# Kernel tuning notes

Measured on AMD Instinct MI355X. Metric: run time of the kernel, lower is better.

## Reference

```python
import jax, jax.numpy as jnp
import numpy as np

N_NODES = 50000


def _gcn_conv(x, src, dst, deg_inv_sqrt, W, b, n_nodes):
    # PyG GCNConv: linear transform, then symmetric-normalized aggregation.
    xw = x @ W  # [N, out_dim]
    norm = deg_inv_sqrt[src] * deg_inv_sqrt[dst]  # [E]
    msg = xw[src] * norm[:, None]  # [E, out_dim] gathered messages
    out = jax.ops.segment_sum(msg, dst, num_segments=n_nodes)
    return out + b


def setup_inputs() -> dict:
    key = jax.random.key(0)
    ks = jax.random.split(key, 10)
    n, d_in, d_h, d_z = N_NODES, 128, 128, 64
    e = 800000
    x = jax.random.normal(ks[0], (n, d_in), dtype=jnp.float32)
    edge_index = jax.random.randint(ks[1], (2, e), 0, n, dtype=jnp.int64)
    eps = jax.random.normal(ks[2], (n, d_z), dtype=jnp.float32)
    s_in = 1.0 / np.sqrt(d_in)
    s_h = 1.0 / np.sqrt(d_h)
    W1 = jax.random.normal(ks[3], (d_in, d_h), dtype=jnp.float32) * s_in
    b1 = jnp.zeros((d_h,), dtype=jnp.float32)
    Wmu = jax.random.normal(ks[4], (d_h, d_z), dtype=jnp.float32) * s_h
    bmu = jnp.zeros((d_z,), dtype=jnp.float32)
    Wls = jax.random.normal(ks[5], (d_h, d_z), dtype=jnp.float32) * s_h
    bls = jnp.zeros((d_z,), dtype=jnp.float32)
    return {"x": x, "edge_index": edge_index, "eps": eps,
            "W1": W1, "b1": b1, "Wmu": Wmu, "bmu": bmu, "Wls": Wls, "bls": bls}


def reference(x, edge_index, eps, W1, b1, Wmu, bmu, Wls, bls):
    n = x.shape[0]
    loops = jnp.arange(n, dtype=edge_index.dtype)
    src = jnp.concatenate([edge_index[0], loops])  # add self-loops
    dst = jnp.concatenate([edge_index[1], loops])
    deg = jax.ops.segment_sum(jnp.ones_like(dst, dtype=x.dtype), dst, num_segments=n)
    deg_inv_sqrt = jnp.where(deg > 0, jax.lax.rsqrt(deg), 0.0)

    hidden = jax.nn.relu(_gcn_conv(x, src, dst, deg_inv_sqrt, W1, b1, n))
    mu = _gcn_conv(hidden, src, dst, deg_inv_sqrt, Wmu, bmu, n)
    logstd = _gcn_conv(hidden, src, dst, deg_inv_sqrt, Wls, bls, n)
    z = mu + eps * jnp.exp(logstd)  # reparameterize (training mode)
    return (z, mu, logstd)
```

## Files before the change

kernel.cpp:

```cpp
#include <hip/hip_runtime.h>
#include <math.h>

#define LDP 136
#define EPB 4096
#define BCAP 8192

typedef short v8s __attribute__((ext_vector_type(8)));
typedef float f32x4 __attribute__((ext_vector_type(4)));

static __device__ __forceinline__ unsigned short f2bf(float f) {
    unsigned u = __builtin_bit_cast(unsigned, f);
    return (unsigned short)((u + 0x7FFFu + ((u >> 16) & 1u)) >> 16);
}
static __device__ __forceinline__ float bf_lo(unsigned u) {
    return __builtin_bit_cast(float, u << 16);
}
static __device__ __forceinline__ float bf_hi(unsigned u) {
    return __builtin_bit_cast(float, u & 0xFFFF0000u);
}

__global__ void prep_w(const float* __restrict__ W1, const float* __restrict__ Wmu,
                       const float* __restrict__ Wls,
                       unsigned short* __restrict__ WT1, unsigned short* __restrict__ WTc,
                       int* __restrict__ ccur, int nb) {
    int i = blockIdx.x * 256 + threadIdx.x;
    if (i < 16384) {
        int j = i >> 7, k = i & 127;
        WT1[i] = f2bf(W1[k * 128 + j]);
    } else if (i < 32768) {
        int i2 = i - 16384;
        int j = i2 >> 7, k = i2 & 127;
        WTc[i2] = f2bf(j < 64 ? Wmu[k * 64 + j] : Wls[k * 64 + (j - 64)]);
    } else {
        int b = i - 32768;
        if (b < nb) ccur[b] = b * BCAP;
    }
}

__global__ __launch_bounds__(256) void part_direct(const int* __restrict__ src,
                                                   const int* __restrict__ dst,
                                                   int* __restrict__ ccur,
                                                   unsigned* __restrict__ pak, int e, int nb) {
    __shared__ int h[256];
    __shared__ int cur[256];
    int t = threadIdx.x;
    h[t] = 0;
    __syncthreads();
    int beg = blockIdx.x * EPB;
    int end = min(e, beg + EPB);
    for (int i = beg + t; i < end; i += 256)
        atomicAdd(&h[dst[i] >> 8], 1);
    __syncthreads();
    if (t < nb) {
        int c = h[t];
        cur[t] = c ? atomicAdd(&ccur[t], c) : 0;
    }
    __syncthreads();
    for (int i = beg + t; i < end; i += 256) {
        int d = dst[i];
        int b = d >> 8;
        int pos = atomicAdd(&cur[b], 1);
        if (pos < (b + 1) * BCAP)
            pak[pos] = (unsigned)src[i] | ((unsigned)(d & 255) << 16);
    }
}

__global__ __launch_bounds__(256) void scan196(const int* __restrict__ ccur,
                                               int* __restrict__ coffs, int nb) {
    __shared__ int buf[256];
    int t = threadIdx.x;
    int v = 0;
    if (t < nb) {
        v = ccur[t] - t * BCAP;
        if (v > BCAP) v = BCAP;
    }
    buf[t] = v;
    __syncthreads();
    for (int off = 1; off < 256; off <<= 1) {
        int add = (t >= off) ? buf[t - off] : 0;
        __syncthreads();
        buf[t] += add;
        __syncthreads();
    }
    if (t < nb) coffs[t] = buf[t] - v;
}

__global__ __launch_bounds__(256) void build_csr(const unsigned* __restrict__ pak,
                                                 const int* __restrict__ ccur,
                                                 const int* __restrict__ coffs,
                                                 int* __restrict__ offs,
                                                 float* __restrict__ dis,
                                                 unsigned short* __restrict__ csr, int n) {
    __shared__ int cnt[256];
    __shared__ int buf[256];
    __shared__ int cur[256];
    int t = threadIdx.x;
    int b = blockIdx.x;
    int ebeg = b * BCAP;
    int eend = min(ccur[b], ebeg + BCAP);
    cnt[t] = 0;
    __syncthreads();
    for (int i = ebeg + t; i < eend; i += 256)
        atomicAdd(&cnt[pak[i] >> 16], 1);
    __syncthreads();
    int v = cnt[t];
    buf[t] = v;
    __syncthreads();
    for (int off = 1; off < 256; off <<= 1) {
        int add = (t >= off) ? buf[t - off] : 0;
        __syncthreads();
        buf[t] += add;
        __syncthreads();
    }
    int start = coffs[b] + buf[t] - v;
    cur[t] = start;
    int node = (b << 8) + t;
    if (node < n) {
        offs[node] = start + v;
        dis[node] = rsqrtf(1.0f + (float)v);
    }
    __syncthreads();
    for (int i = ebeg + t; i < eend; i += 256) {
        unsigned p = pak[i];
        int pos = atomicAdd(&cur[p >> 16], 1);
        csr[pos] = (unsigned short)(p & 0xFFFFu);
    }
}

__global__ __launch_bounds__(256) void gemm1(const float* __restrict__ x,
                                             const unsigned short* __restrict__ WT,
                                             const float* __restrict__ dis,
                                             unsigned short* __restrict__ XWb, int n) {
    __shared__ unsigned short Wt[128 * LDP];
    int t = threadIdx.x;
    {
        const unsigned* Wg = (const unsigned*)WT;
        unsigned* Wl = (unsigned*)Wt;
        for (int i = t; i < 128 * 64; i += 256) {
            int j = i >> 6, k2 = i & 63;
            Wl[j * (LDP / 2) + k2] = Wg[i];
        }
    }
    int lane = t & 63, ww = t >> 6;
    int l15 = lane & 15, quad = lane >> 4;
    int base = blockIdx.x * 64;
    int arow = base + ww * 16 + l15;
    v8s afr[4];
    if (arow < n) {
        const float4* xr = (const float4*)(x + (long)arow * 128);
        #pragma unroll
        for (int kk = 0; kk < 4; ++kk) {
            float4 f0 = xr[kk * 8 + quad * 2];
            float4 f1 = xr[kk * 8 + quad * 2 + 1];
            uint4 p;
            p.x = (unsigned)f2bf(f0.x) | ((unsigned)f2bf(f0.y) << 16);
            p.y = (unsigned)f2bf(f0.z) | ((unsigned)f2bf(f0.w) << 16);
            p.z = (unsigned)f2bf(f1.x) | ((unsigned)f2bf(f1.y) << 16);
            p.w = (unsigned)f2bf(f1.z) | ((unsigned)f2bf(f1.w) << 16);
            afr[kk] = __builtin_bit_cast(v8s, p);
        }
    } else {
        uint4 z = make_uint4(0, 0, 0, 0);
        #pragma unroll
        for (int kk = 0; kk < 4; ++kk) afr[kk] = __builtin_bit_cast(v8s, z);
    }
    __syncthreads();
    f32x4 acc[8];
    #pragma unroll
    for (int i = 0; i < 8; ++i) acc[i] = (f32x4){0.f, 0.f, 0.f, 0.f};
    #pragma unroll
    for (int tt = 0; tt < 8; ++tt) {
        const unsigned short* Brow = Wt + (tt * 16 + l15) * LDP;
        #pragma unroll
        for (int kk = 0; kk < 4; ++kk) {
            uint4 u = *(const uint4*)(Brow + kk * 32 + quad * 8);
            v8s bfr = __builtin_bit_cast(v8s, u);
            acc[tt] = __builtin_amdgcn_mfma_f32_16x16x32_bf16(afr[kk], bfr, acc[tt], 0, 0, 0);
        }
    }
    #pragma unroll
    for (int reg = 0; reg < 4; ++reg) {
        int row = base + ww * 16 + quad * 4 + reg;
        if (row >= n) continue;
        float d = dis[row];
        unsigned short* orow = XWb + (long)row * 128;
        #pragma unroll
        for (int tt = 0; tt < 8; ++tt)
            orow[tt * 16 + l15] = f2bf(acc[tt][reg] * d);
    }
}

__global__ __launch_bounds__(256) void gather128(const unsigned* __restrict__ inb,
                                                 const int* __restrict__ offs,
                                                 const unsigned short* __restrict__ csr,
                                                 const float* __restrict__ dis,
                                                 const float* __restrict__ bias,
                                                 unsigned* __restrict__ outb,
                                                 int n, int mode) {
    int lane = threadIdx.x & 63;
    int i = blockIdx.x * 4 + (threadIdx.x >> 6);
    if (i >= n) return;
    int end = offs[i];
    int beg = (i == 0) ? 0 : offs[i - 1];
    float di = dis[i];
    unsigned su = inb[(long)i * 64 + lane];
    float a0 = bf_lo(su), a1 = bf_hi(su);
    float b0 = 0.f, b1 = 0.f, c0 = 0.f, c1 = 0.f, d0 = 0.f, d1 = 0.f;
    for (int cbeg = beg; cbeg < end; cbeg += 64) {
        int cc = end - cbeg; if (cc > 64) cc = 64;
        int myidx = (lane < cc) ? (int)csr[cbeg + lane] : 0;
        int jj = 0;
        for (; jj + 3 < cc; jj += 4) {
            int sA = __shfl(myidx, jj);
            int sB = __shfl(myidx, jj + 1);
            int sC = __shfl(myidx, jj + 2);
            int sD = __shfl(myidx, jj + 3);
            unsigned uA = inb[(long)sA * 64 + lane];
            unsigned uB = inb[(long)sB * 64 + lane];
            unsigned uC = inb[(long)sC * 64 + lane];
            unsigned uD = inb[(long)sD * 64 + lane];
            a0 += bf_lo(uA); a1 += bf_hi(uA);
            b0 += bf_lo(uB); b1 += bf_hi(uB);
            c0 += bf_lo(uC); c1 += bf_hi(uC);
            d0 += bf_lo(uD); d1 += bf_hi(uD);
        }
        for (; jj < cc; ++jj) {
            int sA = __shfl(myidx, jj);
            unsigned uA = inb[(long)sA * 64 + lane];
            a0 += bf_lo(uA); a1 += bf_hi(uA);
        }
    }
    float r0 = di * ((a0 + b0) + (c0 + d0));
    float r1 = di * ((a1 + b1) + (c1 + d1));
    if (mode) {
        r0 += bias[lane * 2];     r0 = fmaxf(r0, 0.f) * di;
        r1 += bias[lane * 2 + 1]; r1 = fmaxf(r1, 0.f) * di;
    }
    outb[(long)i * 64 + lane] = (unsigned)f2bf(r0) | ((unsigned)f2bf(r1) << 16);
}

__global__ __launch_bounds__(256) void epi(const unsigned* __restrict__ AGGb,
                                           const unsigned short* __restrict__ WTc,
                                           const float* __restrict__ bmu,
                                           const float* __restrict__ bls,
                                           const float* __restrict__ eps,
                                           float* Zo, float* MUo, float* LSo, int n) {
    __shared__ unsigned short Wt[128 * LDP];
    int t = threadIdx.x;
    {
        const unsigned* Wg = (const unsigned*)WTc;
        unsigned* Wl = (unsigned*)Wt;
        for (int i = t; i < 128 * 64; i += 256) {
            int j = i >> 6, k2 = i & 63;
            Wl[j * (LDP / 2) + k2] = Wg[i];
        }
    }
    int lane = t & 63, ww = t >> 6;
    int l15 = lane & 15, quad = lane >> 4;
    int base = blockIdx.x * 64;
    int arow = base + ww * 16 + l15;
    v8s afr[4];
    if (arow < n) {
        const uint4* ar = (const uint4*)(AGGb + (long)arow * 64);
        #pragma unroll
        for (int kk = 0; kk < 4; ++kk)
            afr[kk] = __builtin_bit_cast(v8s, ar[kk * 4 + quad]);
    } else {
        uint4 z = make_uint4(0, 0, 0, 0);
        #pragma unroll
        for (int kk = 0; kk < 4; ++kk) afr[kk] = __builtin_bit_cast(v8s, z);
    }
    __syncthreads();
    f32x4 acc[8];
    #pragma unroll
    for (int i = 0; i < 8; ++i) acc[i] = (f32x4){0.f, 0.f, 0.f, 0.f};
    #pragma unroll
    for (int tt = 0; tt < 8; ++tt) {
        const unsigned short* Brow = Wt + (tt * 16 + l15) * LDP;
        #pragma unroll
        for (int kk = 0; kk < 4; ++kk) {
            uint4 u = *(const uint4*)(Brow + kk * 32 + quad * 8);
            v8s bfr = __builtin_bit_cast(v8s, u);
            acc[tt] = __builtin_amdgcn_mfma_f32_16x16x32_bf16(afr[kk], bfr, acc[tt], 0, 0, 0);
        }
    }
    #pragma unroll
    for (int reg = 0; reg < 4; ++reg) {
        int row = base + ww * 16 + quad * 4 + reg;
        if (row >= n) continue;
        #pragma unroll
        for (int tt = 0; tt < 4; ++tt) {
            int c = tt * 16 + l15;
            long o = (long)row * 64 + c;
            float m = acc[tt][reg] + bmu[c];
            float l = acc[tt + 4][reg] + bls[c];
            Zo[o]  = m + eps[o] * __expf(l);
            MUo[o] = m;
            LSo[o] = l;
        }
    }
}

extern "C" void kernel_launch(void* const* d_in, const int* in_sizes, int n_in,
                              void* d_out, int out_size, void* d_ws, size_t ws_size,
                              hipStream_t stream) {
    const float* x   = (const float*)d_in[0];
    const int*   ei  = (const int*)d_in[1];
    const float* eps = (const float*)d_in[2];
    const float* W1  = (const float*)d_in[3];
    const float* b1  = (const float*)d_in[4];
    const float* Wmu = (const float*)d_in[5];
    const float* bmu = (const float*)d_in[6];
    const float* Wls = (const float*)d_in[7];
    const float* bls = (const float*)d_in[8];

    int n = in_sizes[0] / 128;
    int e = in_sizes[1] / 2;
    const int* src = ei;
    const int* dst = ei + e;
    long nh = (long)n * 64;
    int P = (n + 255) & ~255;
    int NB = (n + 255) >> 8;

    float*          dis   = (float*)d_ws;
    int*            offs  = (int*)(dis + P);
    unsigned short* csr16 = (unsigned short*)(offs + P);
    unsigned short* WT1   = csr16 + ((e + 1) & ~1);
    unsigned short* WTc   = WT1 + 16384;
    int*            ccur  = (int*)(WTc + 16384);
    int*            coffs = ccur + 256;

    float* A = (float*)d_out;
    float* B = A + nh;
    float* C = A + 2 * nh;
    unsigned short* XWb  = (unsigned short*)C;
    unsigned*       Hb   = (unsigned*)A;
    unsigned*       AGGb = (unsigned*)B;
    unsigned*       pak  = (unsigned*)A;

    int gb  = (n + 63) / 64;
    int gbn = (n + 3) / 4;
    int pb  = (e + EPB - 1) / EPB;

    prep_w<<<129, 256, 0, stream>>>(W1, Wmu, Wls, WT1, WTc, ccur, NB);
    part_direct<<<pb, 256, 0, stream>>>(src, dst, ccur, pak, e, NB);
    scan196<<<1, 256, 0, stream>>>(ccur, coffs, NB);
    build_csr<<<NB, 256, 0, stream>>>(pak, ccur, coffs, offs, dis, csr16, n);

    gemm1<<<gb, 256, 0, stream>>>(x, WT1, dis, XWb, n);

    gather128<<<gbn, 256, 0, stream>>>((const unsigned*)XWb, offs, csr16, dis, b1, Hb, n, 1);

    gather128<<<gbn, 256, 0, stream>>>(Hb, offs, csr16, dis, b1, AGGb, n, 0);

    epi<<<gb, 256, 0, stream>>>(AGGb, WTc, bmu, bls, eps, A, B, C, n);
}
```

Baseline: 220.0 us.

## Fuse second aggregation with epilogue GEMM and fold scan into CSR build

Measured after the change: 240.2 us. +9.2%, slower.

```diff
diff --git a/kernel.cpp b/kernel.cpp
--- a/kernel.cpp
+++ b/kernel.cpp
@@ -65,16 +65,24 @@
     }
 }
 
-__global__ __launch_bounds__(256) void scan196(const int* __restrict__ ccur,
-                                               int* __restrict__ coffs, int nb) {
+__global__ __launch_bounds__(256) void build_csr2(const unsigned* __restrict__ pak,
+                                                  const int* __restrict__ ccur,
+                                                  int* __restrict__ offs,
+                                                  float* __restrict__ dis,
+                                                  unsigned short* __restrict__ csr,
+                                                  int n, int nb) {
+    __shared__ int cnt[256];
     __shared__ int buf[256];
+    __shared__ int cur[256];
     int t = threadIdx.x;
-    int v = 0;
+    int b = blockIdx.x;
+    int bc = 0;
     if (t < nb) {
-        v = ccur[t] - t * BCAP;
-        if (v > BCAP) v = BCAP;
-    }
-    buf[t] = v;
+        bc = ccur[t] - t * BCAP;
+        if (bc > BCAP) bc = BCAP;
+        if (bc < 0) bc = 0;
+    }
+    buf[t] = bc;
     __syncthreads();
     for (int off = 1; off < 256; off <<= 1) {
         int add = (t >= off) ? buf[t - off] : 0;
@@ -82,20 +90,7 @@
         buf[t] += add;
         __syncthreads();
     }
-    if (t < nb) coffs[t] = buf[t] - v;
-}
-
-__global__ __launch_bounds__(256) void build_csr(const unsigned* __restrict__ pak,
-                                                 const int* __restrict__ ccur,
-                                                 const int* __restrict__ coffs,
-                                                 int* __restrict__ offs,
-                                                 float* __restrict__ dis,
-                                                 unsigned short* __restrict__ csr, int n) {
-    __shared__ int cnt[256];
-    __shared__ int buf[256];
-    __shared__ int cur[256];
-    int t = threadIdx.x;
-    int b = blockIdx.x;
+    int cbase = (b == 0) ? 0 : buf[b - 1];
     int ebeg = b * BCAP;
     int eend = min(ccur[b], ebeg + BCAP);
     cnt[t] = 0;
@@ -112,7 +107,7 @@
         buf[t] += add;
         __syncthreads();
     }
-    int start = coffs[b] + buf[t] - v;
+    int start = cbase + buf[t] - v;
     cur[t] = start;
     int node = (b << 8) + t;
     if (node < n) {
@@ -239,6 +234,97 @@
     outb[(long)i * 64 + lane] = (unsigned)f2bf(r0) | ((unsigned)f2bf(r1) << 16);
 }
 
+__global__ __launch_bounds__(256) void gather_epi(const unsigned* __restrict__ Hb,
+                                                  const int* __restrict__ offs,
+                                                  const unsigned short* __restrict__ csr,
+                                                  const float* __restrict__ dis,
+                                                  const unsigned short* __restrict__ WTc,
+                                                  const float* __restrict__ bmu,
+                                                  const float* __restrict__ bls,
+                                                  const float* __restrict__ eps,
+                                                  float* Zo, float* MUo, float* LSo, int n) {
+    __shared__ unsigned agg[64][68];
+    int t = threadIdx.x, lane = t & 63, w = t >> 6;
+    int base = blockIdx.x * 64;
+    for (int k = 0; k < 16; ++k) {
+        int i = base + w * 16 + k;
+        unsigned packed = 0;
+        if (i < n) {
+            int end = offs[i];
+            int beg = (i == 0) ? 0 : offs[i - 1];
+            float di = dis[i];
+            unsigned su = Hb[(long)i * 64 + lane];
+            float a0 = bf_lo(su), a1 = bf_hi(su);
+            float b0 = 0.f, b1 = 0.f, c0 = 0.f, c1 = 0.f, d0 = 0.f, d1 = 0.f;
+            for (int cbeg = beg; cbeg < end; cbeg += 64) {
+                int cc = end - cbeg; if (cc > 64) cc = 64;
+                int myidx = (lane < cc) ? (int)csr[cbeg + lane] : 0;
+                int jj = 0;
+                for (; jj + 3 < cc; jj += 4) {
+                    int sA = __shfl(myidx, jj);
+                    int sB = __shfl(myidx, jj + 1);
+                    int sC = __shfl(myidx, jj + 2);
+                    int sD = __shfl(myidx, jj + 3);
+                    unsigned uA = Hb[(long)sA * 64 + lane];
+                    unsigned uB = Hb[(long)sB * 64 + lane];
+                    unsigned uC = Hb[(long)sC * 64 + lane];
+                    unsigned uD = Hb[(long)sD * 64 + lane];
+                    a0 += bf_lo(uA); a1 += bf_hi(uA);
+                    b0 += bf_lo(uB); b1 += bf_hi(uB);
+                    c0 += bf_lo(uC); c1 += bf_hi(uC);
+                    d0 += bf_lo(uD); d1 += bf_hi(uD);
+                }
+                for (; jj < cc; ++jj) {
+                    int sA = __shfl(myidx, jj);
+                    unsigned uA = Hb[(long)sA * 64 + lane];
+                    a0 += bf_lo(uA); a1 += bf_hi(uA);
+                }
+            }
+            float r0 = di * ((a0 + b0) + (c0 + d0));
+            float r1 = di * ((a1 + b1) + (c1 + d1));
+            packed = (unsigned)f2bf(r0) | ((unsigned)f2bf(r1) << 16);
+        }
+        agg[w * 16 + k][lane] = packed;
+    }
+    __syncthreads();
+    int l15 = lane & 15, quad = lane >> 4;
+    v8s afr[4];
+    {
+        const unsigned* ar = &agg[w * 16 + l15][0];
+        #pragma unroll
+        for (int kk = 0; kk < 4; ++kk)
+            afr[kk] = __builtin_bit_cast(v8s, *(const uint4*)(ar + kk * 16 + quad * 4));
+    }
+    f32x4 acc[8];
+    #pragma unroll
+    for (int i = 0; i < 8; ++i) acc[i] = (f32x4){0.f, 0.f, 0.f, 0.f};
+    #pragma unroll
+    for (int tt = 0; tt < 8; ++tt) {
+        const unsigned short* Brow = WTc + (tt * 16 + l15) * 128;
+        #pragma unroll
+        for (int kk = 0; kk < 4; ++kk) {
+            uint4 u = *(const uint4*)(Brow + kk * 32 + quad * 8);
+            v8s bfr = __builtin_bit_cast(v8s, u);
+            acc[tt] = __builtin_amdgcn_mfma_f32_16x16x32_bf16(afr[kk], bfr, acc[tt], 0, 0, 0);
+        }
+    }
+    #pragma unroll
+    for (int reg = 0; reg < 4; ++reg) {
+        int row = base + w * 16 + quad * 4 + reg;
+        if (row >= n) continue;
+        #pragma unroll
+        for (int tt = 0; tt < 4; ++tt) {
+            int c = tt * 16 + l15;
+            long o = (long)row * 64 + c;
+            float m = acc[tt][reg] + bmu[c];
+            float l = acc[tt + 4][reg] + bls[c];
+            Zo[o]  = m + eps[o] * __expf(l);
+            MUo[o] = m;
+            LSo[o] = l;
+        }
+    }
+}
+
 __global__ __launch_bounds__(256) void epi(const unsigned* __restrict__ AGGb,
                                            const unsigned short* __restrict__ WTc,
                                            const float* __restrict__ bmu,
@@ -328,13 +414,16 @@
     unsigned short* WT1   = csr16 + ((e + 1) & ~1);
     unsigned short* WTc   = WT1 + 16384;
     int*            ccur  = (int*)(WTc + 16384);
-    int*            coffs = ccur + 256;
+    char*           hb0   = (char*)(ccur + 256);
+    hb0 = (char*)(((unsigned long long)hb0 + 255ull) & ~255ull);
+    size_t need = (size_t)(hb0 - (char*)d_ws) + (size_t)nh * 4;
+    int fused = (ws_size >= need);
 
     float* A = (float*)d_out;
     float* B = A + nh;
     float* C = A + 2 * nh;
     unsigned short* XWb  = (unsigned short*)C;
-    unsigned*       Hb   = (unsigned*)A;
+    unsigned*       Hb   = fused ? (unsigned*)hb0 : (unsigned*)A;
     unsigned*       AGGb = (unsigned*)B;
     unsigned*       pak  = (unsigned*)A;
 
@@ -344,14 +433,17 @@
 
     prep_w<<<129, 256, 0, stream>>>(W1, Wmu, Wls, WT1, WTc, ccur, NB);
     part_direct<<<pb, 256, 0, stream>>>(src, dst, ccur, pak, e, NB);
-    scan196<<<1, 256, 0, stream>>>(ccur, coffs, NB);
-    build_csr<<<NB, 256, 0, stream>>>(pak, ccur, coffs, offs, dis, csr16, n);
+    build_csr2<<<NB, 256, 0, stream>>>(pak, ccur, offs, dis, csr16, n, NB);
 
     gemm1<<<gb, 256, 0, stream>>>(x, WT1, dis, XWb, n);
 
     gather128<<<gbn, 256, 0, stream>>>((const unsigned*)XWb, offs, csr16, dis, b1, Hb, n, 1);
 
-    gather128<<<gbn, 256, 0, stream>>>(Hb, offs, csr16, dis, b1, AGGb, n, 0);
-
-    epi<<<gb, 256, 0, stream>>>(AGGb, WTc, bmu, bls, eps, A, B, C, n);
-}
+    if (fused) {
+        gather_epi<<<gb, 256, 0, stream>>>(Hb, offs, csr16, dis, WTc, bmu, bls, eps,
+                                           A, B, C, n);
+    } else {
+        gather128<<<gbn, 256, 0, stream>>>(Hb, offs, csr16, dis, b1, AGGb, n, 0);
+        epi<<<gb, 256, 0, stream>>>(AGGb, WTc, bmu, bls, eps, A, B, C, n);
+    }
+}
```
